# Performance work log

Hardware: AMD Instinct MI355X
Metric: run time of the kernel (lower is better)

The kernel has to match this reference:

```python
import jax, jax.numpy as jnp
import numpy as np

N_EMBD = 2048
N_HEAD = 8          # config.n_head // 2
HEAD_DIM = 256      # n_embd // (n_head // 2)
HALF = HEAD_DIM // 2
LAMBDA_INIT = 0.8
RMS_EPS = 1.1920929e-07  # torch float32 finfo eps (F.rms_norm default)


def _rms_norm(x):
    # F.rms_norm with no weight: x / sqrt(mean(x^2) + eps)
    return x * jax.lax.rsqrt(jnp.mean(x * x, axis=-1, keepdims=True) + RMS_EPS)


def setup_inputs() -> dict:
    key = jax.random.key(0)
    ks = jax.random.split(key, 10)
    B, T, C = 2, 2048, N_EMBD
    x = jax.random.normal(ks[0], (B, T, C), dtype=jnp.float32)
    wq = jax.random.normal(ks[1], (C, C), dtype=jnp.float32) * 0.02
    wk = jax.random.normal(ks[2], (C, C), dtype=jnp.float32) * 0.02
    wv = jax.random.normal(ks[3], (C, C), dtype=jnp.float32) * 0.02
    wo = jax.random.normal(ks[4], (C, C), dtype=jnp.float32) * 0.02
    lq1 = jax.random.normal(ks[5], (HEAD_DIM,), dtype=jnp.float32) * 0.1
    lk1 = jax.random.normal(ks[6], (HEAD_DIM,), dtype=jnp.float32) * 0.1
    lq2 = jax.random.normal(ks[7], (HEAD_DIM,), dtype=jnp.float32) * 0.1
    lk2 = jax.random.normal(ks[8], (HEAD_DIM,), dtype=jnp.float32) * 0.1
    return {"x": x, "wq": wq, "wk": wk, "wv": wv, "wo": wo,
            "lq1": lq1, "lk1": lk1, "lq2": lq2, "lk2": lk2}


def _causal_attn(q, k, v, mask):
    # q,k: [B,H,T,half], v: [B,H,T,HEAD_DIM]
    scale = 1.0 / jnp.sqrt(jnp.asarray(q.shape[-1], q.dtype))
    scores = jnp.einsum('bhqd,bhkd->bhqk', q, k) * scale
    scores = jnp.where(mask, scores, -jnp.inf)
    attn = jax.nn.softmax(scores, axis=-1)
    return jnp.einsum('bhqk,bhkd->bhqd', attn, v)


def reference(x, wq, wk, wv, wo, lq1, lk1, lq2, lk2):
    B, T, C = x.shape
    lambda_1 = jnp.exp(jnp.sum(lq1 * lk1))
    lambda_2 = jnp.exp(jnp.sum(lq2 * lk2))
    lambda_full = lambda_1 - lambda_2 + LAMBDA_INIT

    q = (x @ wq.T).reshape(B, T, N_HEAD, 2, HALF).transpose(0, 2, 1, 3, 4)  # [B,H,T,2,half]
    k = (x @ wk.T).reshape(B, T, N_HEAD, 2, HALF).transpose(0, 2, 1, 3, 4)
    v = (x @ wv.T).reshape(B, T, N_HEAD, HEAD_DIM).transpose(0, 2, 1, 3)    # [B,H,T,hd]

    q1 = _rms_norm(q[..., 0, :]); q2 = _rms_norm(q[..., 1, :])
    k1 = _rms_norm(k[..., 0, :]); k2 = _rms_norm(k[..., 1, :])

    mask = jnp.tril(jnp.ones((T, T), dtype=bool))
    y1 = _causal_attn(q1, k1, v, mask)
    y2 = _causal_attn(q2, k2, v, mask)
    y = y1 - lambda_full * y2                                               # [B,H,T,hd]

    y = y.transpose(0, 2, 1, 3).reshape(B, T, C)
    return (y @ wo.T) * (1.0 - LAMBDA_INIT)
```

## Files before the change

### kernel.cpp

```cpp
#include <hip/hip_runtime.h>
#include <stdint.h>


typedef __bf16 bf16;
typedef bf16 bf16x8 __attribute__((ext_vector_type(8)));
typedef bf16 bf16x4 __attribute__((ext_vector_type(4)));
typedef bf16 bf16x2 __attribute__((ext_vector_type(2)));
typedef float f32x4 __attribute__((ext_vector_type(4)));

typedef void __attribute__((address_space(1)))* gas_t;
typedef void __attribute__((address_space(3)))* las_t;

__device__ __forceinline__ void gload16(const void* g, void* l) {
  __builtin_amdgcn_global_load_lds((gas_t)(uintptr_t)g, (las_t)(uint32_t)(uintptr_t)l, 16, 0, 0);
}

__device__ __forceinline__ f32x4 mfma16x16(bf16x8 a, bf16x8 b, f32x4 c) {
  return __builtin_amdgcn_mfma_f32_16x16x32_bf16(a, b, c, 0, 0, 0);
}

__global__ __launch_bounds__(256) void cast_f32_bf16(const float* __restrict__ in,
                                                     bf16* __restrict__ out, int n4) {
  int i = blockIdx.x * 256 + threadIdx.x;
  if (i >= n4) return;
  float4 v = ((const float4*)in)[i];
  bf16x4 o;
  o[0] = (bf16)v.x; o[1] = (bf16)v.y; o[2] = (bf16)v.z; o[3] = (bf16)v.w;
  ((bf16x4*)out)[i] = o;
}

__global__ __launch_bounds__(256) void cast4_w(const float* __restrict__ a, const float* __restrict__ b,
                                               const float* __restrict__ c, const float* __restrict__ d,
                                               bf16* __restrict__ oa, bf16* __restrict__ ob,
                                               bf16* __restrict__ oc, bf16* __restrict__ od) {
  int w = blockIdx.y;
  const float* in = (w == 0) ? a : (w == 1) ? b : (w == 2) ? c : d;
  bf16* out = (w == 0) ? oa : (w == 1) ? ob : (w == 2) ? oc : od;
  int i = blockIdx.x * 256 + threadIdx.x;
  float4 v = ((const float4*)in)[i];
  bf16x4 o;
  o[0] = (bf16)v.x; o[1] = (bf16)v.y; o[2] = (bf16)v.z; o[3] = (bf16)v.w;
  ((bf16x4*)out)[i] = o;
}

__global__ void lambda_kernel(const float* __restrict__ lq1, const float* __restrict__ lk1,
                              const float* __restrict__ lq2, const float* __restrict__ lk2,
                              float* __restrict__ out) {
  __shared__ float red[8];
  int tid = threadIdx.x;
  float a = lq1[tid] * lk1[tid];
  float b = lq2[tid] * lk2[tid];
#pragma unroll
  for (int m = 32; m >= 1; m >>= 1) {
    a += __shfl_xor(a, m, 64);
    b += __shfl_xor(b, m, 64);
  }
  if ((tid & 63) == 0) { red[tid >> 6] = a; red[4 + (tid >> 6)] = b; }
  __syncthreads();
  if (tid == 0) {
    float s1 = red[0] + red[1] + red[2] + red[3];
    float s2 = red[4] + red[5] + red[6] + red[7];
    out[0] = expf(s1) - expf(s2) + 0.8f;
  }
}

template <int MODE>
__global__ __launch_bounds__(256, 2) void gemm_pipe(const bf16* __restrict__ A,
                                                    const bf16* __restrict__ Bq,
                                                    const bf16* __restrict__ Bk,
                                                    const bf16* __restrict__ Bv,
                                                    bf16* __restrict__ Cq, bf16* __restrict__ Ck,
                                                    bf16* __restrict__ Cv,
                                                    float* __restrict__ Cf) {
  __shared__ char lds[73728];
  const int K = 2048, nt = 64;

  int p = blockIdx.y * gridDim.x + blockIdx.x;
  const int nwg = (MODE == 0) ? 768 : 256;
  const int cpx = nwg >> 3;
  int lid = (p & 7) * cpx + (p >> 3);
  const int ntn = (MODE == 0) ? 48 : 16;
  const int bm = (lid / ntn) * 256;
  const int bnG = (lid % ntn) * 128;
  const int z = (MODE == 0) ? (bnG >> 11) : 0;
  const int bn = bnG & 2047;
  const bf16* B = (MODE == 1) ? Bq : ((z == 0) ? Bq : ((z == 1) ? Bk : Bv));

  const int tid = threadIdx.x;
  const int wid = tid >> 6, lane = tid & 63;
  const int l15 = lane & 15, lhi = lane >> 4;
  const int wm = wid >> 1, wn = wid & 1;

  const bf16* aB = A + (size_t)(bm + l15) * K + lhi * 8;
  const bf16* bB = B + (size_t)(bn + l15) * K + lhi * 8;

  auto stage = [&](int t, int pb) {
    char* base = lds + pb * 24576;
    const int k0 = t * 32;
    gload16(aB + (size_t)((0 + wid) * 16) * K + k0, base + wid * 1024);
    gload16(aB + (size_t)((4 + wid) * 16) * K + k0, base + 4096 + wid * 1024);
    gload16(aB + (size_t)((8 + wid) * 16) * K + k0, base + 8192 + wid * 1024);
    gload16(aB + (size_t)((12 + wid) * 16) * K + k0, base + 12288 + wid * 1024);
    gload16(bB + (size_t)((0 + wid) * 16) * K + k0, base + 16384 + wid * 1024);
    gload16(bB + (size_t)((4 + wid) * 16) * K + k0, base + 20480 + wid * 1024);
  };

  const f32x4 fz = {0.f, 0.f, 0.f, 0.f};
  f32x4 acc[8][4];
#pragma unroll
  for (int m = 0; m < 8; ++m)
#pragma unroll
    for (int n = 0; n < 4; ++n) acc[m][n] = fz;

  stage(0, 0);
  stage(1, 1);
  asm volatile("s_waitcnt vmcnt(6)" ::: "memory");
  __builtin_amdgcn_s_barrier();

  for (int t = 0; t < nt; ++t) {
    const char* ab = lds + (t % 3) * 24576;
    if (t + 2 < nt) stage(t + 2, (t + 2) % 3);
    bf16x8 a[8], b[4];
#pragma unroll
    for (int m = 0; m < 8; ++m)
      a[m] = *(const bf16x8*)(ab + (wm * 8 + m) * 1024 + lane * 16);
#pragma unroll
    for (int n = 0; n < 4; ++n)
      b[n] = *(const bf16x8*)(ab + 16384 + (wn * 4 + n) * 1024 + lane * 16);
    __builtin_amdgcn_s_setprio(1);
#pragma unroll
    for (int m = 0; m < 8; ++m)
#pragma unroll
      for (int n = 0; n < 4; ++n) acc[m][n] = mfma16x16(a[m], b[n], acc[m][n]);
    __builtin_amdgcn_s_setprio(0);
    if (t + 2 < nt) {
      asm volatile("s_waitcnt vmcnt(6)" ::: "memory");
    } else {
      asm volatile("s_waitcnt vmcnt(0)" ::: "memory");
    }
    __builtin_amdgcn_s_barrier();
  }

  if (MODE == 1) {
#pragma unroll
    for (int m = 0; m < 8; ++m)
#pragma unroll
      for (int n = 0; n < 4; ++n)
#pragma unroll
        for (int r = 0; r < 4; ++r) {
          int row = bm + wm * 128 + m * 16 + lhi * 4 + r;
          int col = bnG + wn * 64 + n * 16 + l15;
          Cf[(size_t)row * 2048 + col] = acc[m][n][r] * 0.2f;
        }
    return;
  }
  if (z == 2) {
#pragma unroll
    for (int m = 0; m < 8; ++m)
#pragma unroll
      for (int n = 0; n < 4; ++n)
#pragma unroll
        for (int r = 0; r < 4; ++r) {
          int row = bm + wm * 128 + m * 16 + lhi * 4 + r;
          int d = bn + wn * 64 + n * 16 + l15;
          int bb3 = row >> 11, tt = row & 2047;
          Cv[(size_t)bb3 * 2048 * 2048 + (size_t)d * 2048 + tt] = (bf16)acc[m][n][r];
        }
    return;
  }
  float* ldsf = (float*)lds;
#pragma unroll
  for (int m = 0; m < 8; ++m)
#pragma unroll
    for (int r = 0; r < 4; ++r) {
      float s = 0.f;
#pragma unroll
      for (int n = 0; n < 4; ++n) s += acc[m][n][r] * acc[m][n][r];
      s += __shfl_xor(s, 1, 64);
      s += __shfl_xor(s, 2, 64);
      s += __shfl_xor(s, 4, 64);
      s += __shfl_xor(s, 8, 64);
      if (l15 == 0) ldsf[(wm * 128 + m * 16 + lhi * 4 + r) * 2 + wn] = s;
    }
  __syncthreads();
  const float osc = (z == 0) ? 0.08838834764831845f : 1.0f;
  bf16* C = (z == 0) ? Cq : Ck;
#pragma unroll
  for (int m = 0; m < 8; ++m)
#pragma unroll
    for (int r = 0; r < 4; ++r) {
      int rl = wm * 128 + m * 16 + lhi * 4 + r;
      float tot = ldsf[rl * 2] + ldsf[rl * 2 + 1];
      float sc = rsqrtf(tot * (1.0f / 128.0f) + 1.1920929e-07f) * osc;
#pragma unroll
      for (int n = 0; n < 4; ++n) {
        int col = bn + wn * 64 + n * 16 + l15;
        C[(size_t)(bm + rl) * 2048 + col] = (bf16)(acc[m][n][r] * sc);
      }
    }
}

__global__ __launch_bounds__(256) void attn_kernel(const bf16* __restrict__ qb, const bf16* __restrict__ kb,
                                                   const bf16* __restrict__ vtb, bf16* __restrict__ yb,
                                                   const float* __restrict__ lamp) {
  __shared__ char lds[53248];
  const int tid = threadIdx.x;
  const int wid = tid >> 6, lane = tid & 63;
  const int l15 = lane & 15, lhi = lane >> 4;
  char* vtl = lds + 32768;
  char* pbf = lds + 49152 + wid * 1024;
  const int qt = 31 - blockIdx.y;
  const int bh = blockIdx.x;
  const int b = bh >> 3, h = bh & 7;
  const int qr0 = qt * 64 + wid * 16;
  const float lam = lamp[0];

  const bf16* qrow = qb + (size_t)(b * 2048 + qr0 + l15) * 2048 + h * 256 + lhi * 8;
  bf16x8 q1f[4], q2f[4];
#pragma unroll
  for (int s = 0; s < 4; ++s) {
    q1f[s] = *(const bf16x8*)(qrow + s * 32);
    q2f[s] = *(const bf16x8*)(qrow + 128 + s * 32);
  }

  const f32x4 fz = {0.f, 0.f, 0.f, 0.f};
  f32x4 y1[16], y2[16];
#pragma unroll
  for (int f = 0; f < 16; ++f) { y1[f] = fz; y2[f] = fz; }
  float l1[4] = {0.f, 0.f, 0.f, 0.f}, l2[4] = {0.f, 0.f, 0.f, 0.f};

  const int nkt = 2 * qt + 2;
  const bf16* kbase = kb + (size_t)(b * 2048) * 2048 + h * 256;
  const bf16* vbase = vtb + (size_t)b * 2048 * 2048 + (size_t)(h * 256) * 2048;

  auto stageK = [&](int kt2, int p) {
    const int t0 = kt2 * 32;
    char* kd = lds + p * 16384 + wid * 1024;
    const bf16* sp = kbase + (size_t)(t0 + l15) * 2048 + wid * 32 + lhi * 8;
    gload16(sp, kd);
    gload16(sp + 16 * 2048, kd + 4096);
    gload16(sp + 128, kd + 8192);
    gload16(sp + 16 * 2048 + 128, kd + 12288);
  };
  auto stageVT = [&](int kt2) {
    const int t0 = kt2 * 32;
    const bf16* vp = vbase + (size_t)(wid * 16 + l15) * 2048 + t0 + lhi * 8;
#pragma unroll
    for (int i = 0; i < 4; ++i)
      gload16(vp + (size_t)i * 64 * 2048, vtl + (i * 4 + wid) * 1024);
  };

  stageK(0, 0);
  stageVT(0);
  __syncthreads();

  for (int kt = 0; kt < nkt; ++kt) {
    const int cur = kt & 1;
    const int t0 = kt * 32;
    const bool active = (t0 <= qr0 + 15);
    f32x4 s1g[2], s2g[2];
    if (active) {
      const char* kc = lds + cur * 16384;
#pragma unroll
      for (int g = 0; g < 2; ++g) {
        f32x4 a1 = fz, a2 = fz;
#pragma unroll
        for (int s = 0; s < 4; ++s) {
          a1 = mfma16x16(q1f[s], *(const bf16x8*)(kc + ((g * 4 + s) * 64 + lane) * 16), a1);
          a2 = mfma16x16(q2f[s], *(const bf16x8*)(kc + 8192 + ((g * 4 + s) * 64 + lane) * 16), a2);
        }
        s1g[g] = a1;
        s2g[g] = a2;
      }
      if (t0 + 31 > qr0) {
#pragma unroll
        for (int g = 0; g < 2; ++g) {
          int col = t0 + g * 16 + l15;
#pragma unroll
          for (int r = 0; r < 4; ++r) {
            int row = qr0 + lhi * 4 + r;
            if (col > row) { s1g[g][r] = -1e30f; s2g[g][r] = -1e30f; }
          }
        }
      }
#pragma unroll
      for (int g = 0; g < 2; ++g) {
#pragma unroll
        for (int r = 0; r < 4; ++r) {
          float p1 = __expf(s1g[g][r] - 12.0f);
          float p2 = __expf(s2g[g][r] - 12.0f);
          l1[r] += p1;
          l2[r] += p2;
          *(bf16*)(pbf + ((lhi * 4 + r) * 32 + g * 16 + l15) * 2) = (bf16)p1;
          s2g[g][r] = p2;
        }
      }
    }
    __syncthreads();
    if (active) {
      bf16x8 pa1 = *(const bf16x8*)(pbf + (l15 * 32 + lhi * 8) * 2);
#pragma unroll
      for (int f = 0; f < 16; ++f)
        y1[f] = mfma16x16(pa1, *(const bf16x8*)(vtl + (f * 64 + lane) * 16), y1[f]);
#pragma unroll
      for (int g = 0; g < 2; ++g)
#pragma unroll
        for (int r = 0; r < 4; ++r)
          *(bf16*)(pbf + ((lhi * 4 + r) * 32 + g * 16 + l15) * 2) = (bf16)s2g[g][r];
      bf16x8 pa2 = *(const bf16x8*)(pbf + (l15 * 32 + lhi * 8) * 2);
#pragma unroll
      for (int f = 0; f < 16; ++f)
        y2[f] = mfma16x16(pa2, *(const bf16x8*)(vtl + (f * 64 + lane) * 16), y2[f]);
    }
    __syncthreads();
    if (kt + 1 < nkt) {
      stageK(kt + 1, cur ^ 1);
      stageVT(kt + 1);
    }
  }

#pragma unroll
  for (int r = 0; r < 4; ++r) {
    float s1 = l1[r], s2 = l2[r];
#pragma unroll
    for (int m = 1; m <= 8; m <<= 1) {
      s1 += __shfl_xor(s1, m, 64);
      s2 += __shfl_xor(s2, m, 64);
    }
    float inv1 = 1.f / s1;
    float inv2 = lam / s2;
    int row = qr0 + lhi * 4 + r;
    bf16* orow = yb + (size_t)(b * 2048 + row) * 2048 + h * 256 + l15;
#pragma unroll
    for (int f = 0; f < 16; ++f) {
      float v = y1[f][r] * inv1 - y2[f][r] * inv2;
      orow[f * 16] = (bf16)v;
    }
  }
}

extern "C" void kernel_launch(void* const* d_in, const int* in_sizes, int n_in,
                              void* d_out, int out_size, void* d_ws, size_t ws_size,
                              hipStream_t stream) {
  const float* x = (const float*)d_in[0];
  const float* wq = (const float*)d_in[1];
  const float* wk = (const float*)d_in[2];
  const float* wv = (const float*)d_in[3];
  const float* wo = (const float*)d_in[4];
  const float* lq1 = (const float*)d_in[5];
  const float* lk1 = (const float*)d_in[6];
  const float* lq2 = (const float*)d_in[7];
  const float* lk2 = (const float*)d_in[8];
  float* out = (float*)d_out;
  char* ws = (char*)d_ws;

  if (ws_size < 117440516) return;

  bf16* xb = (bf16*)(ws + 0);
  bf16* wqb = (bf16*)(ws + 16777216);
  bf16* wkb = (bf16*)(ws + 25165824);
  bf16* wvb = (bf16*)(ws + 33554432);
  bf16* wob = (bf16*)(ws + 41943040);
  bf16* qbuf = (bf16*)(ws + 50331648);
  bf16* kbuf = (bf16*)(ws + 67108864);
  bf16* vtb = (bf16*)(ws + 83886080);
  bf16* ybuf = (bf16*)(ws + 100663296);
  float* lam = (float*)(ws + 117440512);

  cast_f32_bf16<<<8192, 256, 0, stream>>>(x, xb, 2097152);
  cast4_w<<<dim3(4096, 4), 256, 0, stream>>>(wq, wk, wv, wo, wqb, wkb, wvb, wob);
  lambda_kernel<<<1, 256, 0, stream>>>(lq1, lk1, lq2, lk2, lam);

  gemm_pipe<0><<<dim3(48, 16), 256, 0, stream>>>(xb, wqb, wkb, wvb, qbuf, kbuf, vtb, nullptr);

  attn_kernel<<<dim3(16, 32), 256, 0, stream>>>(qbuf, kbuf, vtb, ybuf, lam);

  gemm_pipe<1><<<dim3(16, 16), 256, 0, stream>>>(ybuf, wob, nullptr, nullptr, nullptr, nullptr, nullptr, out);
}
```

Measured before the change: 359.5 us.

## Use 256x256 tiles with 8 waves and split-phase staging for QKV GEMM

```diff
diff --git a/kernel.cpp b/kernel.cpp
--- a/kernel.cpp
+++ b/kernel.cpp
@@ -64,27 +64,154 @@
   }
 }
 
-template <int MODE>
-__global__ __launch_bounds__(256, 2) void gemm_pipe(const bf16* __restrict__ A,
+__global__ __launch_bounds__(512, 2) void gemm_qkv8(const bf16* __restrict__ A,
                                                     const bf16* __restrict__ Bq,
                                                     const bf16* __restrict__ Bk,
                                                     const bf16* __restrict__ Bv,
                                                     bf16* __restrict__ Cq, bf16* __restrict__ Ck,
-                                                    bf16* __restrict__ Cv,
-                                                    float* __restrict__ Cf) {
+                                                    bf16* __restrict__ Cv) {
+  __shared__ char lds[98304];
+  const int K = 2048, nt = 64;
+
+  int p = blockIdx.y * gridDim.x + blockIdx.x;
+  int lid = (p & 7) * 48 + (p >> 3);
+  const int bm = (lid / 24) * 256;
+  const int bnG = (lid % 24) * 256;
+  const int z = bnG >> 11;
+  const int bn = bnG & 2047;
+  const bf16* B = (z == 0) ? Bq : ((z == 1) ? Bk : Bv);
+
+  const int tid = threadIdx.x;
+  const int wid = tid >> 6, lane = tid & 63;
+  const int l15 = lane & 15, lhi = lane >> 4;
+  const int wm = wid >> 2, wn = wid & 3;
+
+  const bf16* aS0 = A + (size_t)(bm + wid * 16 + l15) * K + lhi * 8;
+  const bf16* bS0 = B + (size_t)(bn + wid * 16 + l15) * K + lhi * 8;
+
+  auto stA = [&](int t, int pb) {
+    char* d = lds + pb * 32768 + wid * 1024;
+    const bf16* s = aS0 + t * 32;
+    gload16(s, d);
+    gload16(s + (size_t)128 * K, d + 8192);
+  };
+  auto stB = [&](int t, int pb) {
+    char* d = lds + pb * 32768 + 16384 + wid * 1024;
+    const bf16* s = bS0 + t * 32;
+    gload16(s, d);
+    gload16(s + (size_t)128 * K, d + 8192);
+  };
+
+  const f32x4 fz = {0.f, 0.f, 0.f, 0.f};
+  f32x4 acc[8][4];
+#pragma unroll
+  for (int m = 0; m < 8; ++m)
+#pragma unroll
+    for (int n = 0; n < 4; ++n) acc[m][n] = fz;
+
+  stA(0, 0); stB(0, 0);
+  stA(1, 1); stB(1, 1);
+  asm volatile("s_waitcnt vmcnt(4)" ::: "memory");
+  __builtin_amdgcn_s_barrier();
+
+  int cur = 0;
+  for (int t = 0; t < nt; ++t) {
+    const char* ab = lds + cur * 32768;
+    const char* bb = ab + 16384;
+    int nx2 = cur + 2; if (nx2 >= 3) nx2 -= 3;
+    bf16x8 a[8], b0, b1;
+
+#pragma unroll
+    for (int m = 0; m < 8; ++m) a[m] = *(const bf16x8*)(ab + (wm * 8 + m) * 1024 + lane * 16);
+    b0 = *(const bf16x8*)(bb + (wn * 4 + 0) * 1024 + lane * 16);
+    b1 = *(const bf16x8*)(bb + (wn * 4 + 1) * 1024 + lane * 16);
+    if (t + 2 < nt) stA(t + 2, nx2);
+    __builtin_amdgcn_s_barrier();
+    __builtin_amdgcn_s_setprio(1);
+#pragma unroll
+    for (int m = 0; m < 8; ++m) {
+      acc[m][0] = mfma16x16(a[m], b0, acc[m][0]);
+      acc[m][1] = mfma16x16(a[m], b1, acc[m][1]);
+    }
+    __builtin_amdgcn_s_setprio(0);
+    __builtin_amdgcn_s_barrier();
+
+    b0 = *(const bf16x8*)(bb + (wn * 4 + 2) * 1024 + lane * 16);
+    b1 = *(const bf16x8*)(bb + (wn * 4 + 3) * 1024 + lane * 16);
+    if (t + 2 < nt) stB(t + 2, nx2);
+    __builtin_amdgcn_s_barrier();
+    __builtin_amdgcn_s_setprio(1);
+#pragma unroll
+    for (int m = 0; m < 8; ++m) {
+      acc[m][2] = mfma16x16(a[m], b0, acc[m][2]);
+      acc[m][3] = mfma16x16(a[m], b1, acc[m][3]);
+    }
+    __builtin_amdgcn_s_setprio(0);
+    if (t + 2 < nt) {
+      asm volatile("s_waitcnt vmcnt(4)" ::: "memory");
+    } else {
+      asm volatile("s_waitcnt vmcnt(0)" ::: "memory");
+    }
+    __builtin_amdgcn_s_barrier();
+
+    cur = (cur == 2) ? 0 : cur + 1;
+  }
+
+  if (z == 2) {
+#pragma unroll
+    for (int m = 0; m < 8; ++m)
+#pragma unroll
+      for (int n = 0; n < 4; ++n)
+#pragma unroll
+        for (int r = 0; r < 4; ++r) {
+          int row = bm + wm * 128 + m * 16 + lhi * 4 + r;
+          int col = bn + wn * 64 + n * 16 + l15;
+          int bb3 = row >> 11, tt = row & 2047;
+          Cv[(size_t)bb3 * 2048 * 2048 + (size_t)col * 2048 + tt] = (bf16)acc[m][n][r];
+        }
+    return;
+  }
+  float* ldsf = (float*)lds;
+#pragma unroll
+  for (int m = 0; m < 8; ++m)
+#pragma unroll
+    for (int r = 0; r < 4; ++r) {
+      float s = acc[m][0][r] * acc[m][0][r] + acc[m][1][r] * acc[m][1][r] +
+                acc[m][2][r] * acc[m][2][r] + acc[m][3][r] * acc[m][3][r];
+      s += __shfl_xor(s, 1, 64);
+      s += __shfl_xor(s, 2, 64);
+      s += __shfl_xor(s, 4, 64);
+      s += __shfl_xor(s, 8, 64);
+      if (l15 == 0) ldsf[(wm * 128 + m * 16 + lhi * 4 + r) * 4 + wn] = s;
+    }
+  __syncthreads();
+  const float osc = (z == 0) ? 0.08838834764831845f : 1.0f;
+  bf16* C = (z == 0) ? Cq : Ck;
+#pragma unroll
+  for (int m = 0; m < 8; ++m) {
+#pragma unroll
+    for (int r = 0; r < 4; ++r) {
+      int rl = wm * 128 + m * 16 + lhi * 4 + r;
+      float tot = ldsf[rl * 4 + (wn & 2)] + ldsf[rl * 4 + (wn & 2) + 1];
+      float sc = rsqrtf(tot * (1.0f / 128.0f) + 1.1920929e-07f) * osc;
+#pragma unroll
+      for (int n = 0; n < 4; ++n) {
+        int col = bn + wn * 64 + n * 16 + l15;
+        C[(size_t)(bm + rl) * 2048 + col] = (bf16)(acc[m][n][r] * sc);
+      }
+    }
+  }
+}
+
+__global__ __launch_bounds__(256, 2) void gemm_out(const bf16* __restrict__ A, const bf16* __restrict__ B,
+                                                   float* __restrict__ Cf) {
   __shared__ char lds[73728];
   const int K = 2048, nt = 64;
 
   int p = blockIdx.y * gridDim.x + blockIdx.x;
-  const int nwg = (MODE == 0) ? 768 : 256;
-  const int cpx = nwg >> 3;
-  int lid = (p & 7) * cpx + (p >> 3);
-  const int ntn = (MODE == 0) ? 48 : 16;
-  const int bm = (lid / ntn) * 256;
-  const int bnG = (lid % ntn) * 128;
-  const int z = (MODE == 0) ? (bnG >> 11) : 0;
-  const int bn = bnG & 2047;
-  const bf16* B = (MODE == 1) ? Bq : ((z == 0) ? Bq : ((z == 1) ? Bk : Bv));
+  int lid = (p & 7) * 32 + (p >> 3);
+  const int bm = (lid / 16) * 256;
+  const int bn = (lid % 16) * 128;
 
   const int tid = threadIdx.x;
   const int wid = tid >> 6, lane = tid & 63;
@@ -141,63 +268,16 @@
     __builtin_amdgcn_s_barrier();
   }
 
-  if (MODE == 1) {
-#pragma unroll
-    for (int m = 0; m < 8; ++m)
-#pragma unroll
-      for (int n = 0; n < 4; ++n)
-#pragma unroll
-        for (int r = 0; r < 4; ++r) {
-          int row = bm + wm * 128 + m * 16 + lhi * 4 + r;
-          int col = bnG + wn * 64 + n * 16 + l15;
-          Cf[(size_t)row * 2048 + col] = acc[m][n][r] * 0.2f;
-        }
-    return;
-  }
-  if (z == 2) {
-#pragma unroll
-    for (int m = 0; m < 8; ++m)
-#pragma unroll
-      for (int n = 0; n < 4; ++n)
-#pragma unroll
-        for (int r = 0; r < 4; ++r) {
-          int row = bm + wm * 128 + m * 16 + lhi * 4 + r;
-          int d = bn + wn * 64 + n * 16 + l15;
-          int bb3 = row >> 11, tt = row & 2047;
-          Cv[(size_t)bb3 * 2048 * 2048 + (size_t)d * 2048 + tt] = (bf16)acc[m][n][r];
-        }
-    return;
-  }
-  float* ldsf = (float*)lds;
 #pragma unroll
   for (int m = 0; m < 8; ++m)
 #pragma unroll
-    for (int r = 0; r < 4; ++r) {
-      float s = 0.f;
-#pragma unroll
-      for (int n = 0; n < 4; ++n) s += acc[m][n][r] * acc[m][n][r];
-      s += __shfl_xor(s, 1, 64);
-      s += __shfl_xor(s, 2, 64);
-      s += __shfl_xor(s, 4, 64);
-      s += __shfl_xor(s, 8, 64);
-      if (l15 == 0) ldsf[(wm * 128 + m * 16 + lhi * 4 + r) * 2 + wn] = s;
-    }
-  __syncthreads();
-  const float osc = (z == 0) ? 0.08838834764831845f : 1.0f;
-  bf16* C = (z == 0) ? Cq : Ck;
-#pragma unroll
-  for (int m = 0; m < 8; ++m)
-#pragma unroll
-    for (int r = 0; r < 4; ++r) {
-      int rl = wm * 128 + m * 16 + lhi * 4 + r;
-      float tot = ldsf[rl * 2] + ldsf[rl * 2 + 1];
-      float sc = rsqrtf(tot * (1.0f / 128.0f) + 1.1920929e-07f) * osc;
-#pragma unroll
-      for (int n = 0; n < 4; ++n) {
+    for (int n = 0; n < 4; ++n)
+#pragma unroll
+      for (int r = 0; r < 4; ++r) {
+        int row = bm + wm * 128 + m * 16 + lhi * 4 + r;
         int col = bn + wn * 64 + n * 16 + l15;
-        C[(size_t)(bm + rl) * 2048 + col] = (bf16)(acc[m][n][r] * sc);
+        Cf[(size_t)row * 2048 + col] = acc[m][n][r] * 0.2f;
       }
-    }
 }
 
 __global__ __launch_bounds__(256) void attn_kernel(const bf16* __restrict__ qb, const bf16* __restrict__ kb,
@@ -371,9 +451,9 @@
   cast4_w<<<dim3(4096, 4), 256, 0, stream>>>(wq, wk, wv, wo, wqb, wkb, wvb, wob);
   lambda_kernel<<<1, 256, 0, stream>>>(lq1, lk1, lq2, lk2, lam);
 
-  gemm_pipe<0><<<dim3(48, 16), 256, 0, stream>>>(xb, wqb, wkb, wvb, qbuf, kbuf, vtb, nullptr);
+  gemm_qkv8<<<dim3(24, 16), 512, 0, stream>>>(xb, wqb, wkb, wvb, qbuf, kbuf, vtb);
 
   attn_kernel<<<dim3(16, 32), 256, 0, stream>>>(qbuf, kbuf, vtb, ybuf, lam);
 
-  gemm_pipe<1><<<dim3(16, 16), 256, 0, stream>>>(ybuf, wob, nullptr, nullptr, nullptr, nullptr, nullptr, out);
-}
+  gemm_out<<<dim3(16, 16), 256, 0, stream>>>(ybuf, wob, out);
+}
```

Result: faster. 350.6 us (-2.5%).

## Reshape GEMM tiles to 128x256 with per-wave column split and interleaved staging

Applied to the files above, without the earlier changes.

```diff
diff --git a/kernel.cpp b/kernel.cpp
--- a/kernel.cpp
+++ b/kernel.cpp
@@ -79,9 +79,9 @@
   const int nwg = (MODE == 0) ? 768 : 256;
   const int cpx = nwg >> 3;
   int lid = (p & 7) * cpx + (p >> 3);
-  const int ntn = (MODE == 0) ? 48 : 16;
-  const int bm = (lid / ntn) * 256;
-  const int bnG = (lid % ntn) * 128;
+  const int ntn = (MODE == 0) ? 24 : 8;
+  const int bm = (lid / ntn) * 128;
+  const int bnG = (lid % ntn) * 256;
   const int z = (MODE == 0) ? (bnG >> 11) : 0;
   const int bn = bnG & 2047;
   const bf16* B = (MODE == 1) ? Bq : ((z == 0) ? Bq : ((z == 1) ? Bk : Bv));
@@ -89,20 +89,27 @@
   const int tid = threadIdx.x;
   const int wid = tid >> 6, lane = tid & 63;
   const int l15 = lane & 15, lhi = lane >> 4;
-  const int wm = wid >> 1, wn = wid & 1;
-
-  const bf16* aB = A + (size_t)(bm + l15) * K + lhi * 8;
-  const bf16* bB = B + (size_t)(bn + l15) * K + lhi * 8;
-
-  auto stage = [&](int t, int pb) {
-    char* base = lds + pb * 24576;
-    const int k0 = t * 32;
-    gload16(aB + (size_t)((0 + wid) * 16) * K + k0, base + wid * 1024);
-    gload16(aB + (size_t)((4 + wid) * 16) * K + k0, base + 4096 + wid * 1024);
-    gload16(aB + (size_t)((8 + wid) * 16) * K + k0, base + 8192 + wid * 1024);
-    gload16(aB + (size_t)((12 + wid) * 16) * K + k0, base + 12288 + wid * 1024);
-    gload16(bB + (size_t)((0 + wid) * 16) * K + k0, base + 16384 + wid * 1024);
-    gload16(bB + (size_t)((4 + wid) * 16) * K + k0, base + 20480 + wid * 1024);
+
+  const bf16* aS0 = A + (size_t)(bm + wid * 16 + l15) * K + lhi * 8;
+  const bf16* bS0 = B + (size_t)(bn + wid * 16 + l15) * K + lhi * 8;
+
+  auto stA = [&](int t, int pb) {
+    char* d = lds + pb * 24576 + wid * 1024;
+    const bf16* s = aS0 + t * 32;
+    gload16(s, d);
+    gload16(s + (size_t)64 * K, d + 4096);
+  };
+  auto stBlo = [&](int t, int pb) {
+    char* d = lds + pb * 24576 + 8192 + wid * 1024;
+    const bf16* s = bS0 + t * 32;
+    gload16(s, d);
+    gload16(s + (size_t)64 * K, d + 4096);
+  };
+  auto stBhi = [&](int t, int pb) {
+    char* d = lds + pb * 24576 + 8192 + (wid + 8) * 1024;
+    const bf16* s = bS0 + t * 32;
+    gload16(s + (size_t)128 * K, d);
+    gload16(s + (size_t)192 * K, d + 4096);
   };
 
   const f32x4 fz = {0.f, 0.f, 0.f, 0.f};
@@ -112,26 +119,42 @@
 #pragma unroll
     for (int n = 0; n < 4; ++n) acc[m][n] = fz;
 
-  stage(0, 0);
-  stage(1, 1);
+  stA(0, 0); stBlo(0, 0); stBhi(0, 0);
+  stA(1, 1); stBlo(1, 1); stBhi(1, 1);
   asm volatile("s_waitcnt vmcnt(6)" ::: "memory");
   __builtin_amdgcn_s_barrier();
 
+  int cur = 0;
   for (int t = 0; t < nt; ++t) {
-    const char* ab = lds + (t % 3) * 24576;
-    if (t + 2 < nt) stage(t + 2, (t + 2) % 3);
-    bf16x8 a[8], b[4];
-#pragma unroll
-    for (int m = 0; m < 8; ++m)
-      a[m] = *(const bf16x8*)(ab + (wm * 8 + m) * 1024 + lane * 16);
-#pragma unroll
-    for (int n = 0; n < 4; ++n)
-      b[n] = *(const bf16x8*)(ab + 16384 + (wn * 4 + n) * 1024 + lane * 16);
+    const char* ab = lds + cur * 24576;
+    int nx2 = cur + 2; if (nx2 >= 3) nx2 -= 3;
+    bf16x8 a[8], b0, b1;
+
+#pragma unroll
+    for (int m = 0; m < 8; ++m) a[m] = *(const bf16x8*)(ab + m * 1024 + lane * 16);
+    b0 = *(const bf16x8*)(ab + 8192 + (wid * 4 + 0) * 1024 + lane * 16);
+    b1 = *(const bf16x8*)(ab + 8192 + (wid * 4 + 1) * 1024 + lane * 16);
+    if (t + 2 < nt) { stA(t + 2, nx2); stBlo(t + 2, nx2); }
+    __builtin_amdgcn_s_barrier();
     __builtin_amdgcn_s_setprio(1);
 #pragma unroll
-    for (int m = 0; m < 8; ++m)
-#pragma unroll
-      for (int n = 0; n < 4; ++n) acc[m][n] = mfma16x16(a[m], b[n], acc[m][n]);
+    for (int m = 0; m < 8; ++m) {
+      acc[m][0] = mfma16x16(a[m], b0, acc[m][0]);
+      acc[m][1] = mfma16x16(a[m], b1, acc[m][1]);
+    }
+    __builtin_amdgcn_s_setprio(0);
+    __builtin_amdgcn_s_barrier();
+
+    b0 = *(const bf16x8*)(ab + 8192 + (wid * 4 + 2) * 1024 + lane * 16);
+    b1 = *(const bf16x8*)(ab + 8192 + (wid * 4 + 3) * 1024 + lane * 16);
+    if (t + 2 < nt) stBhi(t + 2, nx2);
+    __builtin_amdgcn_s_barrier();
+    __builtin_amdgcn_s_setprio(1);
+#pragma unroll
+    for (int m = 0; m < 8; ++m) {
+      acc[m][2] = mfma16x16(a[m], b0, acc[m][2]);
+      acc[m][3] = mfma16x16(a[m], b1, acc[m][3]);
+    }
     __builtin_amdgcn_s_setprio(0);
     if (t + 2 < nt) {
       asm volatile("s_waitcnt vmcnt(6)" ::: "memory");
@@ -139,6 +162,8 @@
       asm volatile("s_waitcnt vmcnt(0)" ::: "memory");
     }
     __builtin_amdgcn_s_barrier();
+
+    cur = (cur == 2) ? 0 : cur + 1;
   }
 
   if (MODE == 1) {
@@ -148,8 +173,8 @@
       for (int n = 0; n < 4; ++n)
 #pragma unroll
         for (int r = 0; r < 4; ++r) {
-          int row = bm + wm * 128 + m * 16 + lhi * 4 + r;
-          int col = bnG + wn * 64 + n * 16 + l15;
+          int row = bm + m * 16 + lhi * 4 + r;
+          int col = bnG + wid * 64 + n * 16 + l15;
           Cf[(size_t)row * 2048 + col] = acc[m][n][r] * 0.2f;
         }
     return;
@@ -161,8 +186,8 @@
       for (int n = 0; n < 4; ++n)
 #pragma unroll
         for (int r = 0; r < 4; ++r) {
-          int row = bm + wm * 128 + m * 16 + lhi * 4 + r;
-          int d = bn + wn * 64 + n * 16 + l15;
+          int row = bm + m * 16 + lhi * 4 + r;
+          int d = bn + wid * 64 + n * 16 + l15;
           int bb3 = row >> 11, tt = row & 2047;
           Cv[(size_t)bb3 * 2048 * 2048 + (size_t)d * 2048 + tt] = (bf16)acc[m][n][r];
         }
@@ -180,7 +205,7 @@
       s += __shfl_xor(s, 2, 64);
       s += __shfl_xor(s, 4, 64);
       s += __shfl_xor(s, 8, 64);
-      if (l15 == 0) ldsf[(wm * 128 + m * 16 + lhi * 4 + r) * 2 + wn] = s;
+      if (l15 == 0) ldsf[(m * 16 + lhi * 4 + r) * 4 + wid] = s;
     }
   __syncthreads();
   const float osc = (z == 0) ? 0.08838834764831845f : 1.0f;
@@ -189,12 +214,12 @@
   for (int m = 0; m < 8; ++m)
 #pragma unroll
     for (int r = 0; r < 4; ++r) {
-      int rl = wm * 128 + m * 16 + lhi * 4 + r;
-      float tot = ldsf[rl * 2] + ldsf[rl * 2 + 1];
+      int rl = m * 16 + lhi * 4 + r;
+      float tot = ldsf[rl * 4 + (wid & 2)] + ldsf[rl * 4 + (wid & 2) + 1];
       float sc = rsqrtf(tot * (1.0f / 128.0f) + 1.1920929e-07f) * osc;
 #pragma unroll
       for (int n = 0; n < 4; ++n) {
-        int col = bn + wn * 64 + n * 16 + l15;
+        int col = bn + wid * 64 + n * 16 + l15;
         C[(size_t)(bm + rl) * 2048 + col] = (bf16)(acc[m][n][r] * sc);
       }
     }
@@ -371,9 +396,9 @@
   cast4_w<<<dim3(4096, 4), 256, 0, stream>>>(wq, wk, wv, wo, wqb, wkb, wvb, wob);
   lambda_kernel<<<1, 256, 0, stream>>>(lq1, lk1, lq2, lk2, lam);
 
-  gemm_pipe<0><<<dim3(48, 16), 256, 0, stream>>>(xb, wqb, wkb, wvb, qbuf, kbuf, vtb, nullptr);
+  gemm_pipe<0><<<dim3(24, 32), 256, 0, stream>>>(xb, wqb, wkb, wvb, qbuf, kbuf, vtb, nullptr);
 
   attn_kernel<<<dim3(16, 32), 256, 0, stream>>>(qbuf, kbuf, vtb, ybuf, lam);
 
-  gemm_pipe<1><<<dim3(16, 16), 256, 0, stream>>>(ybuf, wob, nullptr, nullptr, nullptr, nullptr, nullptr, out);
-}
+  gemm_pipe<1><<<dim3(8, 32), 256, 0, stream>>>(ybuf, wob, nullptr, nullptr, nullptr, nullptr, nullptr, out);
+}
```

Measured after the change: 359.6 us. About the same (+0.0%).

## Retile GEMM to 128x256 blocks with double buffering and per-XCD column mapping

Applied to the files above, without the earlier changes.

```diff
diff --git a/kernel.cpp b/kernel.cpp
--- a/kernel.cpp
+++ b/kernel.cpp
@@ -65,23 +65,22 @@
 }
 
 template <int MODE>
-__global__ __launch_bounds__(256, 2) void gemm_pipe(const bf16* __restrict__ A,
+__global__ __launch_bounds__(256, 3) void gemm_pipe(const bf16* __restrict__ A,
                                                     const bf16* __restrict__ Bq,
                                                     const bf16* __restrict__ Bk,
                                                     const bf16* __restrict__ Bv,
                                                     bf16* __restrict__ Cq, bf16* __restrict__ Ck,
                                                     bf16* __restrict__ Cv,
                                                     float* __restrict__ Cf) {
-  __shared__ char lds[73728];
+  __shared__ char lds[49152];
   const int K = 2048, nt = 64;
 
-  int p = blockIdx.y * gridDim.x + blockIdx.x;
-  const int nwg = (MODE == 0) ? 768 : 256;
-  const int cpx = nwg >> 3;
-  int lid = (p & 7) * cpx + (p >> 3);
-  const int ntn = (MODE == 0) ? 48 : 16;
-  const int bm = (lid / ntn) * 256;
-  const int bnG = (lid % ntn) * 128;
+  const int p = blockIdx.x;
+  const int xcd = p & 7, loc = p >> 3;
+  const int bn_idx = (MODE == 0) ? (xcd * 3 + loc / 32) : xcd;
+  const int bm_idx = (MODE == 0) ? (loc % 32) : loc;
+  const int bm = bm_idx * 128;
+  const int bnG = bn_idx * 256;
   const int z = (MODE == 0) ? (bnG >> 11) : 0;
   const int bn = bnG & 2047;
   const bf16* B = (MODE == 1) ? Bq : ((z == 0) ? Bq : ((z == 1) ? Bk : Bv));
@@ -89,20 +88,20 @@
   const int tid = threadIdx.x;
   const int wid = tid >> 6, lane = tid & 63;
   const int l15 = lane & 15, lhi = lane >> 4;
-  const int wm = wid >> 1, wn = wid & 1;
-
-  const bf16* aB = A + (size_t)(bm + l15) * K + lhi * 8;
-  const bf16* bB = B + (size_t)(bn + l15) * K + lhi * 8;
+
+  const bf16* aS0 = A + (size_t)(bm + wid * 16 + l15) * K + lhi * 8;
+  const bf16* bS0 = B + (size_t)(bn + wid * 16 + l15) * K + lhi * 8;
 
   auto stage = [&](int t, int pb) {
     char* base = lds + pb * 24576;
-    const int k0 = t * 32;
-    gload16(aB + (size_t)((0 + wid) * 16) * K + k0, base + wid * 1024);
-    gload16(aB + (size_t)((4 + wid) * 16) * K + k0, base + 4096 + wid * 1024);
-    gload16(aB + (size_t)((8 + wid) * 16) * K + k0, base + 8192 + wid * 1024);
-    gload16(aB + (size_t)((12 + wid) * 16) * K + k0, base + 12288 + wid * 1024);
-    gload16(bB + (size_t)((0 + wid) * 16) * K + k0, base + 16384 + wid * 1024);
-    gload16(bB + (size_t)((4 + wid) * 16) * K + k0, base + 20480 + wid * 1024);
+    const bf16* sa = aS0 + t * 32;
+    const bf16* sb = bS0 + t * 32;
+    gload16(sa, base + wid * 1024);
+    gload16(sa + (size_t)64 * K, base + 4096 + wid * 1024);
+    gload16(sb, base + 8192 + wid * 1024);
+    gload16(sb + (size_t)64 * K, base + 8192 + 4096 + wid * 1024);
+    gload16(sb + (size_t)128 * K, base + 8192 + (wid + 8) * 1024);
+    gload16(sb + (size_t)192 * K, base + 8192 + (wid + 12) * 1024);
   };
 
   const f32x4 fz = {0.f, 0.f, 0.f, 0.f};
@@ -113,31 +112,25 @@
     for (int n = 0; n < 4; ++n) acc[m][n] = fz;
 
   stage(0, 0);
-  stage(1, 1);
-  asm volatile("s_waitcnt vmcnt(6)" ::: "memory");
+  asm volatile("s_waitcnt vmcnt(0)" ::: "memory");
   __builtin_amdgcn_s_barrier();
 
   for (int t = 0; t < nt; ++t) {
-    const char* ab = lds + (t % 3) * 24576;
-    if (t + 2 < nt) stage(t + 2, (t + 2) % 3);
+    const char* ab = lds + (t & 1) * 24576;
+    if (t + 1 < nt) stage(t + 1, (t + 1) & 1);
     bf16x8 a[8], b[4];
 #pragma unroll
-    for (int m = 0; m < 8; ++m)
-      a[m] = *(const bf16x8*)(ab + (wm * 8 + m) * 1024 + lane * 16);
+    for (int m = 0; m < 8; ++m) a[m] = *(const bf16x8*)(ab + m * 1024 + lane * 16);
 #pragma unroll
     for (int n = 0; n < 4; ++n)
-      b[n] = *(const bf16x8*)(ab + 16384 + (wn * 4 + n) * 1024 + lane * 16);
+      b[n] = *(const bf16x8*)(ab + 8192 + (wid * 4 + n) * 1024 + lane * 16);
     __builtin_amdgcn_s_setprio(1);
 #pragma unroll
     for (int m = 0; m < 8; ++m)
 #pragma unroll
       for (int n = 0; n < 4; ++n) acc[m][n] = mfma16x16(a[m], b[n], acc[m][n]);
     __builtin_amdgcn_s_setprio(0);
-    if (t + 2 < nt) {
-      asm volatile("s_waitcnt vmcnt(6)" ::: "memory");
-    } else {
-      asm volatile("s_waitcnt vmcnt(0)" ::: "memory");
-    }
+    asm volatile("s_waitcnt vmcnt(0)" ::: "memory");
     __builtin_amdgcn_s_barrier();
   }
 
@@ -148,8 +141,8 @@
       for (int n = 0; n < 4; ++n)
 #pragma unroll
         for (int r = 0; r < 4; ++r) {
-          int row = bm + wm * 128 + m * 16 + lhi * 4 + r;
-          int col = bnG + wn * 64 + n * 16 + l15;
+          int row = bm + m * 16 + lhi * 4 + r;
+          int col = bnG + wid * 64 + n * 16 + l15;
           Cf[(size_t)row * 2048 + col] = acc[m][n][r] * 0.2f;
         }
     return;
@@ -161,8 +154,8 @@
       for (int n = 0; n < 4; ++n)
 #pragma unroll
         for (int r = 0; r < 4; ++r) {
-          int row = bm + wm * 128 + m * 16 + lhi * 4 + r;
-          int d = bn + wn * 64 + n * 16 + l15;
+          int row = bm + m * 16 + lhi * 4 + r;
+          int d = bn + wid * 64 + n * 16 + l15;
           int bb3 = row >> 11, tt = row & 2047;
           Cv[(size_t)bb3 * 2048 * 2048 + (size_t)d * 2048 + tt] = (bf16)acc[m][n][r];
         }
@@ -180,7 +173,7 @@
       s += __shfl_xor(s, 2, 64);
       s += __shfl_xor(s, 4, 64);
       s += __shfl_xor(s, 8, 64);
-      if (l15 == 0) ldsf[(wm * 128 + m * 16 + lhi * 4 + r) * 2 + wn] = s;
+      if (l15 == 0) ldsf[(m * 16 + lhi * 4 + r) * 4 + wid] = s;
     }
   __syncthreads();
   const float osc = (z == 0) ? 0.08838834764831845f : 1.0f;
@@ -189,12 +182,12 @@
   for (int m = 0; m < 8; ++m)
 #pragma unroll
     for (int r = 0; r < 4; ++r) {
-      int rl = wm * 128 + m * 16 + lhi * 4 + r;
-      float tot = ldsf[rl * 2] + ldsf[rl * 2 + 1];
+      int rl = m * 16 + lhi * 4 + r;
+      float tot = ldsf[rl * 4 + (wid & 2)] + ldsf[rl * 4 + (wid & 2) + 1];
       float sc = rsqrtf(tot * (1.0f / 128.0f) + 1.1920929e-07f) * osc;
 #pragma unroll
       for (int n = 0; n < 4; ++n) {
-        int col = bn + wn * 64 + n * 16 + l15;
+        int col = bn + wid * 64 + n * 16 + l15;
         C[(size_t)(bm + rl) * 2048 + col] = (bf16)(acc[m][n][r] * sc);
       }
     }
@@ -371,9 +364,9 @@
   cast4_w<<<dim3(4096, 4), 256, 0, stream>>>(wq, wk, wv, wo, wqb, wkb, wvb, wob);
   lambda_kernel<<<1, 256, 0, stream>>>(lq1, lk1, lq2, lk2, lam);
 
-  gemm_pipe<0><<<dim3(48, 16), 256, 0, stream>>>(xb, wqb, wkb, wvb, qbuf, kbuf, vtb, nullptr);
+  gemm_pipe<0><<<768, 256, 0, stream>>>(xb, wqb, wkb, wvb, qbuf, kbuf, vtb, nullptr);
 
   attn_kernel<<<dim3(16, 32), 256, 0, stream>>>(qbuf, kbuf, vtb, ybuf, lam);
 
-  gemm_pipe<1><<<dim3(16, 16), 256, 0, stream>>>(ybuf, wob, nullptr, nullptr, nullptr, nullptr, nullptr, out);
-}
+  gemm_pipe<1><<<256, 256, 0, stream>>>(ybuf, wob, nullptr, nullptr, nullptr, nullptr, nullptr, out);
+}
```

Result: slower. 561.5 us (+56.2%).
